# Optimization experiments

Hardware: AMD Instinct MI355X
Metric: run time of the kernel (lower is better)

The kernel has to match this reference:

```python
import jax, jax.numpy as jnp
import numpy as np

HID = 16
DATA_DIM = 2
B = 2048
T = 64
RTOL, ATOL = 1e-2, 1e-4
SAFETY, FMIN, FMAX = 0.9, 0.2, 10.0
MAX_STEPS = 16  # bounded adaptive-step budget (masked once t reaches T1)
T1 = 1.0
DT0 = 1.0

# Tsit5 (Tsitouras 2011) tableau
_A2 = (0.161,)
_A3 = (-0.008480655492356989, 0.335480655492357)
_A4 = (2.8971530571054935, -6.359448489975075, 4.3622954328695815)
_A5 = (5.325864828439257, -11.748883564062828, 7.4955393428898365, -0.09249506636175525)
_A6 = (5.86145544294642, -12.92096931784711, 8.159367898576159, -0.071584973281401, -0.028269050394068383)
_B5 = (0.09646076681806523, 0.01, 0.4798896504144996, 1.379008574103742, -3.290069515436081, 2.324710524099774)
_BT = (-0.00178001105222577714, -0.0008164344596567469, 0.007880878010261995, -0.1447110071732629, 0.5823571654525552, -0.45808210592918697, 0.015151515151515152)


def setup_inputs() -> dict:
    key = jax.random.key(0)
    ks = jax.random.split(key, 13)
    u = lambda k, shape, fan: jax.random.uniform(k, shape, jnp.float32, -1.0, 1.0) / np.float32(np.sqrt(fan))
    return dict(
        x_seq=jax.random.normal(ks[0], (B, T, DATA_DIM), jnp.float32),
        w1=u(ks[1], (HID, HID), HID), b1=u(ks[2], (HID,), HID),
        w2=u(ks[3], (HID, HID), HID), b2=u(ks[4], (HID,), HID),
        w3=u(ks[5], (HID, HID), HID), b3=u(ks[6], (HID,), HID),
        gru_wih=u(ks[7], (3 * HID, DATA_DIM), DATA_DIM),
        gru_whh=u(ks[8], (3 * HID, HID), HID),
        gru_b=u(ks[9], (3 * HID,), HID),
        gru_bn=u(ks[10], (HID,), HID),
        pred_w=u(ks[11], (1, HID), HID),
        pred_b=u(ks[12], (1,), HID),
    )


def _mlp(y, w1, b1, w2, b2, w3, b3):
    # eqx.nn.MLP(in=16, out=16, width=16, depth=2, activation=tanh): 3 Linear layers
    y = jnp.tanh(y @ w1.T + b1)
    y = jnp.tanh(y @ w2.T + b2)
    return y @ w3.T + b3


def _ode_solve(h0, f):
    """Adaptive Tsit5 + I-controller (diffrax PIDController defaults) from t=0 to t=1.
    Per-sample adaptive step/accept/reject, batched over the leading axis."""
    nB = h0.shape[0]

    def body(state, _):
        y, t, dt = state                      # y:[B,16]  t,dt:[B]
        dt_c = jnp.minimum(dt, T1 - t)        # clip so we never overshoot t1
        d = dt_c[:, None]
        k1 = f(y)
        k2 = f(y + d * (_A2[0] * k1))
        k3 = f(y + d * (_A3[0] * k1 + _A3[1] * k2))
        k4 = f(y + d * (_A4[0] * k1 + _A4[1] * k2 + _A4[2] * k3))
        k5 = f(y + d * (_A5[0] * k1 + _A5[1] * k2 + _A5[2] * k3 + _A5[3] * k4))
        k6 = f(y + d * (_A6[0] * k1 + _A6[1] * k2 + _A6[2] * k3 + _A6[3] * k4 + _A6[4] * k5))
        y_new = y + d * (_B5[0] * k1 + _B5[1] * k2 + _B5[2] * k3 + _B5[3] * k4 + _B5[4] * k5 + _B5[5] * k6)
        k7 = f(y_new)                          # FSAL stage, enters only the error estimate
        err = d * (_BT[0] * k1 + _BT[1] * k2 + _BT[2] * k3 + _BT[3] * k4 + _BT[4] * k5 + _BT[5] * k6 + _BT[6] * k7)
        scale = ATOL + RTOL * jnp.maximum(jnp.abs(y), jnp.abs(y_new))
        err2 = jnp.maximum(jnp.mean((err / scale) ** 2, axis=-1), 1e-16)  # squared RMS norm, [B]
        accept = err2 <= 1.0
        y = jnp.where(accept[:, None], y_new, y)
        t = jnp.where(accept, t + dt_c, t)
        # I-controller: factor = safety * err_norm**(-1/order), order=5
        factor = jnp.clip(SAFETY * err2 ** (-0.1), FMIN, FMAX)
        dt = dt_c * factor
        return (y, t, dt), None

    init = (h0, jnp.zeros((nB,), h0.dtype), jnp.full((nB,), DT0, h0.dtype))
    (y, _, _), _ = jax.lax.scan(body, init, None, length=MAX_STEPS)
    return y


def _gru(x, h, wih, whh, b, bn):
    # eqx.nn.GRUCell math
    ig = x @ wih.T + b
    hg = h @ whh.T
    ir, iz, inn = jnp.split(ig, 3, axis=-1)
    hr, hz, hn = jnp.split(hg, 3, axis=-1)
    r = jax.nn.sigmoid(ir + hr)
    z = jax.nn.sigmoid(iz + hz)
    n = jnp.tanh(inn + r * (hn + bn))
    return n + z * (h - n)


def reference(x_seq, w1, b1, w2, b2, w3, b3, gru_wih, gru_whh, gru_b, gru_bn, pred_w, pred_b):
    f = lambda y: _mlp(y, w1, b1, w2, b2, w3, b3)
    h0 = jnp.zeros((x_seq.shape[0], HID), x_seq.dtype)

    def step(h, x_t):
        h_ev = _ode_solve(h, f)
        h_new = _gru(x_t, h_ev, gru_wih, gru_whh, gru_b, gru_bn)
        return h_new, None

    xs = jnp.swapaxes(x_seq, 0, 1)  # [T, B, D]
    h_final, _ = jax.lax.scan(step, h0, xs)
    return h_final @ pred_w.T + pred_b  # [B, 1]
```

## Files before the change

### kernel.cpp

```cpp
#include <hip/hip_runtime.h>


#define T_STEPS 64
#define NB 2048
#define N_ODE_STEPS 16

typedef float v2f __attribute__((ext_vector_type(2)));

__device__ __forceinline__ v2f make2(float a, float b) { v2f r; r.x = a; r.y = b; return r; }

#define ROR(x, r) __int_as_float(__builtin_amdgcn_update_dpp( \
    0, __float_as_int(x), 0x120 + (r), 0xF, 0xF, true))

__device__ __forceinline__ float rsum16(float v) {
  v += ROR(v, 8);
  v += ROR(v, 4);
  v += ROR(v, 2);
  v += ROR(v, 1);
  return v;
}

__constant__ int PR_[8] = {0, 2, 4, 6, 1, 3, 5, 7};

__device__ __forceinline__ void gather8(float y, v2f (&G)[4]) {
  float r0 = y;
  float r4 = ROR(r0, 4);
  float r2 = ROR(r0, 2);
  float r6 = ROR(r4, 2);
  float r1 = ROR(r0, 1);
  float r3 = ROR(r2, 1);
  float r5 = ROR(r4, 1);
  float r7 = ROR(r6, 1);
  G[0] = make2(r0, r2);
  G[1] = make2(r4, r6);
  G[2] = make2(r1, r3);
  G[3] = make2(r5, r7);
}

__device__ __forceinline__ float dotAB(const v2f (&WA)[4], const v2f (&WB)[4],
                                       const v2f (&G)[4], float bias) {
  v2f a0 = __builtin_elementwise_fma(G[0], WA[0], make2(bias, 0.0f));
  v2f a1 = G[1] * WA[1];
  v2f b0 = G[0] * WB[0];
  v2f b1 = G[1] * WB[1];
  a0 = __builtin_elementwise_fma(G[2], WA[2], a0);
  a1 = __builtin_elementwise_fma(G[3], WA[3], a1);
  b0 = __builtin_elementwise_fma(G[2], WB[2], b0);
  b1 = __builtin_elementwise_fma(G[3], WB[3], b1);
  v2f as = a0 + a1;
  v2f bs = b0 + b1;
  float bsc = bs.x + bs.y;
  float bsw = ROR(bsc, 8);
  return (as.x + as.y) + bsw;
}

__device__ __forceinline__ float fast_tanh(float x) {
  float e = __builtin_amdgcn_exp2f(x * 2.885390081777927f);
  return fmaf(-2.0f, __builtin_amdgcn_rcpf(e + 1.0f), 1.0f);
}

__device__ __forceinline__ float sigmoid_(float x) {
  float e = __builtin_amdgcn_exp2f(x * -1.4426950408889634f);
  return __builtin_amdgcn_rcpf(1.0f + e);
}

__device__ __forceinline__ float mlp_f(float u,
    const v2f (&w1a)[4], const v2f (&w1b)[4], float b1v,
    const v2f (&w2a)[4], const v2f (&w2b)[4], float b2v,
    const v2f (&w3a)[4], const v2f (&w3b)[4], float b3v) {
  v2f G[4];
  gather8(u, G);
  float h1 = fast_tanh(dotAB(w1a, w1b, G, b1v));
  gather8(h1, G);
  float h2 = fast_tanh(dotAB(w2a, w2b, G, b2v));
  gather8(h2, G);
  return dotAB(w3a, w3b, G, b3v);
}

__global__
__attribute__((amdgpu_flat_work_group_size(64, 64), amdgpu_waves_per_eu(1, 1)))
void odern_kernel(
    const float* __restrict__ x_seq,
    const float* __restrict__ w1, const float* __restrict__ b1,
    const float* __restrict__ w2, const float* __restrict__ b2,
    const float* __restrict__ w3, const float* __restrict__ b3,
    const float* __restrict__ gru_wih, const float* __restrict__ gru_whh,
    const float* __restrict__ gru_b, const float* __restrict__ gru_bn,
    const float* __restrict__ pred_w, const float* __restrict__ pred_b,
    float* __restrict__ out) {
  const int tid = threadIdx.x;
  const int j = tid & 15;
  const int g = tid >> 4;
  const int b = blockIdx.x * 4 + g;
  const int jj = (j + 8) & 15;

  v2f w1a[4], w1b[4], w2a[4], w2b[4], w3a[4], w3b[4];
  v2f wha[4], whb[4], wza[4], wzb[4], wna[4], wnb[4];
#pragma unroll
  for (int p = 0; p < 4; ++p) {
    const int ia = (j - PR_[2 * p]) & 15;
    const int ib = (j - PR_[2 * p + 1]) & 15;
    w1a[p] = make2(w1[j * 16 + ia],  w1[j * 16 + ib]);
    w1b[p] = make2(w1[jj * 16 + ia], w1[jj * 16 + ib]);
    w2a[p] = make2(w2[j * 16 + ia],  w2[j * 16 + ib]);
    w2b[p] = make2(w2[jj * 16 + ia], w2[jj * 16 + ib]);
    w3a[p] = make2(w3[j * 16 + ia],  w3[j * 16 + ib]);
    w3b[p] = make2(w3[jj * 16 + ia], w3[jj * 16 + ib]);
    wha[p] = make2(gru_whh[j * 16 + ia],         gru_whh[j * 16 + ib]);
    whb[p] = make2(gru_whh[jj * 16 + ia],        gru_whh[jj * 16 + ib]);
    wza[p] = make2(gru_whh[(16 + j) * 16 + ia],  gru_whh[(16 + j) * 16 + ib]);
    wzb[p] = make2(gru_whh[(16 + jj) * 16 + ia], gru_whh[(16 + jj) * 16 + ib]);
    wna[p] = make2(gru_whh[(32 + j) * 16 + ia],  gru_whh[(32 + j) * 16 + ib]);
    wnb[p] = make2(gru_whh[(32 + jj) * 16 + ia], gru_whh[(32 + jj) * 16 + ib]);
  }
  const float b1v = b1[j], b2v = b2[j], b3v = b3[j];
  const float wih_r0 = gru_wih[j * 2],        wih_r1 = gru_wih[j * 2 + 1];
  const float wih_z0 = gru_wih[(16 + j) * 2], wih_z1 = gru_wih[(16 + j) * 2 + 1];
  const float wih_n0 = gru_wih[(32 + j) * 2], wih_n1 = gru_wih[(32 + j) * 2 + 1];
  const float gb_r = gru_b[j], gb_z = gru_b[16 + j], gb_n = gru_b[32 + j];
  const float bnv = gru_bn[j];
  const float pwv = pred_w[j], pbv = pred_b[0];

  const float* xp = x_seq + (size_t)b * (T_STEPS * 2);

  float h = 0.0f;
#pragma unroll 1
  for (int t = 0; t < T_STEPS; ++t) {
    const float x0 = xp[2 * t];
    const float x1 = xp[2 * t + 1];

    float y = h;
    float tt = 0.0f, dt = 1.0f;
    float k1 = mlp_f(y, w1a, w1b, b1v, w2a, w2b, b2v, w3a, w3b, b3v);
#pragma unroll 1
    for (int s = 0; s < N_ODE_STEPS; ++s) {
      if (__all(tt >= 1.0f)) break;

      const float dt_c = fminf(dt, 1.0f - tt);
      const float d = dt_c;

      float s2 = 0.161f * k1;
      float k2 = mlp_f(fmaf(d, s2, y), w1a, w1b, b1v, w2a, w2b, b2v, w3a, w3b, b3v);

      float s3 = fmaf(0.335480655492357f, k2, -0.008480655492356989f * k1);
      float k3 = mlp_f(fmaf(d, s3, y), w1a, w1b, b1v, w2a, w2b, b2v, w3a, w3b, b3v);

      float s4 = fmaf(4.3622954328695815f, k3,
                 fmaf(-6.359448489975075f, k2, 2.8971530571054935f * k1));
      float k4 = mlp_f(fmaf(d, s4, y), w1a, w1b, b1v, w2a, w2b, b2v, w3a, w3b, b3v);

      float s5 = fmaf(-0.09249506636175525f, k4,
                 fmaf(7.4955393428898365f, k3,
                 fmaf(-11.748883564062828f, k2, 5.325864828439257f * k1)));
      float k5 = mlp_f(fmaf(d, s5, y), w1a, w1b, b1v, w2a, w2b, b2v, w3a, w3b, b3v);

      float s6 = fmaf(-0.028269050394068383f, k5,
                 fmaf(-0.071584973281401f, k4,
                 fmaf(8.159367898576159f, k3,
                 fmaf(-12.92096931784711f, k2, 5.86145544294642f * k1))));
      float k6 = mlp_f(fmaf(d, s6, y), w1a, w1b, b1v, w2a, w2b, b2v, w3a, w3b, b3v);

      float sy = fmaf(2.324710524099774f, k6,
                 fmaf(-3.290069515436081f, k5,
                 fmaf(1.379008574103742f, k4,
                 fmaf(0.4798896504144996f, k3,
                 fmaf(0.01f, k2, 0.09646076681806523f * k1)))));
      float y_new = fmaf(d, sy, y);

      float k7 = mlp_f(y_new, w1a, w1b, b1v, w2a, w2b, b2v, w3a, w3b, b3v);

      float se = fmaf(0.015151515151515152f, k7,
                 fmaf(-0.45808210592918697f, k6,
                 fmaf(0.5823571654525552f, k5,
                 fmaf(-0.1447110071732629f, k4,
                 fmaf(0.007880878010261995f, k3,
                 fmaf(-0.0008164344596567469f, k2, -0.001780011052225777f * k1))))));
      float err = d * se;

      float scale = fmaf(0.01f, fmaxf(fabsf(y), fabsf(y_new)), 0.0001f);
      float r = err * __builtin_amdgcn_rcpf(scale);
      float m = rsum16(r * r) * 0.0625f;
      float err2 = fmaxf(m, 1e-16f);

      const bool acc = err2 <= 1.0f;
      y = acc ? y_new : y;
      tt = acc ? tt + dt_c : tt;
      k1 = acc ? k7 : k1;

      float fac = 0.9f * __builtin_amdgcn_exp2f(-0.1f * __builtin_amdgcn_logf(err2));
      fac = fminf(fmaxf(fac, 0.2f), 10.0f);
      dt = dt_c * fac;
    }

    float ir = fmaf(wih_r1, x1, fmaf(wih_r0, x0, gb_r));
    float iz = fmaf(wih_z1, x1, fmaf(wih_z0, x0, gb_z));
    float in_ = fmaf(wih_n1, x1, fmaf(wih_n0, x0, gb_n));
    v2f G[4];
    gather8(y, G);
    float pre_r = dotAB(wha, whb, G, ir);
    float pre_z = dotAB(wza, wzb, G, iz);
    float hnb   = dotAB(wna, wnb, G, bnv);
    float rg = sigmoid_(pre_r);
    float zg = sigmoid_(pre_z);
    float ng = fast_tanh(fmaf(rg, hnb, in_));
    h = fmaf(zg, y - ng, ng);
  }

  float ps = rsum16(h * pwv);
  if (j == 0) out[b] = ps + pbv;
}

extern "C" void kernel_launch(void* const* d_in, const int* in_sizes, int n_in,
                              void* d_out, int out_size, void* d_ws, size_t ws_size,
                              hipStream_t stream) {
  (void)in_sizes; (void)n_in; (void)out_size; (void)d_ws; (void)ws_size;
  odern_kernel<<<dim3(NB / 4), dim3(64), 0, stream>>>(
      (const float*)d_in[0],
      (const float*)d_in[1], (const float*)d_in[2],
      (const float*)d_in[3], (const float*)d_in[4],
      (const float*)d_in[5], (const float*)d_in[6],
      (const float*)d_in[7], (const float*)d_in[8],
      (const float*)d_in[9], (const float*)d_in[10],
      (const float*)d_in[11], (const float*)d_in[12],
      (float*)d_out);
}
```

Baseline: 177.2 us.

## Split each sample's hidden dot products across two wave halves via permlane32 swap

Each sample now occupies 32 lanes instead of 16, so every lane does half of each 16-wide dot product (4 gathered inputs instead of 8). The halves are combined with a permlane32 swap and a DPP row rotate, and biases are zeroed on the upper half. The grid doubles to 1024 blocks of two samples each. This shortens the per-lane serial chain of DPP gathers and FMAs on the latency-bound ODE path, at the cost of twice as many waves and extra cross-half exchange instructions.

```diff
diff --git a/kernel.cpp b/kernel.cpp
--- a/kernel.cpp
+++ b/kernel.cpp
@@ -6,11 +6,15 @@
 #define N_ODE_STEPS 16
 
 typedef float v2f __attribute__((ext_vector_type(2)));
+typedef int v2i __attribute__((ext_vector_type(2)));
 
 __device__ __forceinline__ v2f make2(float a, float b) { v2f r; r.x = a; r.y = b; return r; }
 
 #define ROR(x, r) __int_as_float(__builtin_amdgcn_update_dpp( \
     0, __float_as_int(x), 0x120 + (r), 0xF, 0xF, true))
+
+#define ROR4_HI(x) __int_as_float(__builtin_amdgcn_update_dpp( \
+    __float_as_int(x), __float_as_int(x), 0x124, 0xC, 0xF, false))
 
 __device__ __forceinline__ float rsum16(float v) {
   v += ROR(v, 8);
@@ -20,38 +24,37 @@
   return v;
 }
 
-__constant__ int PR_[8] = {0, 2, 4, 6, 1, 3, 5, 7};
-
-__device__ __forceinline__ void gather8(float y, v2f (&G)[4]) {
-  float r0 = y;
-  float r4 = ROR(r0, 4);
-  float r2 = ROR(r0, 2);
-  float r6 = ROR(r4, 2);
-  float r1 = ROR(r0, 1);
+__device__ __forceinline__ float xhalf_sum(float part) {
+  v2i pr = __builtin_amdgcn_permlane32_swap(
+      __float_as_int(part), __float_as_int(part), false, false);
+  return __int_as_float(pr[0]) + __int_as_float(pr[1]);
+}
+
+struct G2 { v2f a, b; };
+
+__device__ __forceinline__ G2 gather4(float x) {
+  float r1 = ROR(x, 1);
+  float r2 = ROR(x, 2);
   float r3 = ROR(r2, 1);
-  float r5 = ROR(r4, 1);
-  float r7 = ROR(r6, 1);
-  G[0] = make2(r0, r2);
-  G[1] = make2(r4, r6);
-  G[2] = make2(r1, r3);
-  G[3] = make2(r5, r7);
-}
-
-__device__ __forceinline__ float dotAB(const v2f (&WA)[4], const v2f (&WB)[4],
-                                       const v2f (&G)[4], float bias) {
-  v2f a0 = __builtin_elementwise_fma(G[0], WA[0], make2(bias, 0.0f));
-  v2f a1 = G[1] * WA[1];
-  v2f b0 = G[0] * WB[0];
-  v2f b1 = G[1] * WB[1];
-  a0 = __builtin_elementwise_fma(G[2], WA[2], a0);
-  a1 = __builtin_elementwise_fma(G[3], WA[3], a1);
-  b0 = __builtin_elementwise_fma(G[2], WB[2], b0);
-  b1 = __builtin_elementwise_fma(G[3], WB[3], b1);
-  v2f as = a0 + a1;
-  v2f bs = b0 + b1;
-  float bsc = bs.x + bs.y;
-  float bsw = ROR(bsc, 8);
-  return (as.x + as.y) + bsw;
+  G2 g; g.a = make2(x, r1); g.b = make2(r2, r3); return g;
+}
+
+__device__ __forceinline__ float dotG(const v2f (&WA)[2], const v2f (&WB)[2],
+                                      const G2& g, float seed) {
+  v2f aa = __builtin_elementwise_fma(g.a, WA[0], make2(seed, 0.0f));
+  v2f bb = g.a * WB[0];
+  aa = __builtin_elementwise_fma(g.b, WA[1], aa);
+  bb = __builtin_elementwise_fma(g.b, WB[1], bb);
+  float a  = aa.x + aa.y;
+  float bs = bb.x + bb.y;
+  float part = a + ROR(bs, 8);
+  return ROR4_HI(xhalf_sum(part));
+}
+
+__device__ __forceinline__ float dotAB(const v2f (&WA)[2], const v2f (&WB)[2],
+                                       float x, float seed) {
+  G2 g = gather4(x);
+  return dotG(WA, WB, g, seed);
 }
 
 __device__ __forceinline__ float fast_tanh(float x) {
@@ -65,16 +68,12 @@
 }
 
 __device__ __forceinline__ float mlp_f(float u,
-    const v2f (&w1a)[4], const v2f (&w1b)[4], float b1v,
-    const v2f (&w2a)[4], const v2f (&w2b)[4], float b2v,
-    const v2f (&w3a)[4], const v2f (&w3b)[4], float b3v) {
-  v2f G[4];
-  gather8(u, G);
-  float h1 = fast_tanh(dotAB(w1a, w1b, G, b1v));
-  gather8(h1, G);
-  float h2 = fast_tanh(dotAB(w2a, w2b, G, b2v));
-  gather8(h2, G);
-  return dotAB(w3a, w3b, G, b3v);
+    const v2f (&w1a)[2], const v2f (&w1b)[2], float b1s,
+    const v2f (&w2a)[2], const v2f (&w2b)[2], float b2s,
+    const v2f (&w3a)[2], const v2f (&w3b)[2], float b3s) {
+  float h1 = fast_tanh(dotAB(w1a, w1b, u, b1s));
+  float h2 = fast_tanh(dotAB(w2a, w2b, h1, b2s));
+  return dotAB(w3a, w3b, h2, b3s);
 }
 
 __global__
@@ -90,48 +89,58 @@
     float* __restrict__ out) {
   const int tid = threadIdx.x;
   const int j = tid & 15;
-  const int g = tid >> 4;
-  const int b = blockIdx.x * 4 + g;
+  const int row16 = tid >> 4;
+  const int smp = row16 & 1;
+  const int hf = row16 >> 1;
+  const int b = blockIdx.x * 2 + smp;
   const int jj = (j + 8) & 15;
-
-  v2f w1a[4], w1b[4], w2a[4], w2b[4], w3a[4], w3b[4];
-  v2f wha[4], whb[4], wza[4], wzb[4], wna[4], wnb[4];
+  const int base = (j - 4 * hf) & 15;
+
+  v2f w1a[2], w1b[2], w2a[2], w2b[2], w3a[2], w3b[2];
+  v2f wha[2], whb[2], wza[2], wzb[2], wna[2], wnb[2];
 #pragma unroll
-  for (int p = 0; p < 4; ++p) {
-    const int ia = (j - PR_[2 * p]) & 15;
-    const int ib = (j - PR_[2 * p + 1]) & 15;
-    w1a[p] = make2(w1[j * 16 + ia],  w1[j * 16 + ib]);
-    w1b[p] = make2(w1[jj * 16 + ia], w1[jj * 16 + ib]);
-    w2a[p] = make2(w2[j * 16 + ia],  w2[j * 16 + ib]);
-    w2b[p] = make2(w2[jj * 16 + ia], w2[jj * 16 + ib]);
-    w3a[p] = make2(w3[j * 16 + ia],  w3[j * 16 + ib]);
-    w3b[p] = make2(w3[jj * 16 + ia], w3[jj * 16 + ib]);
-    wha[p] = make2(gru_whh[j * 16 + ia],         gru_whh[j * 16 + ib]);
-    whb[p] = make2(gru_whh[jj * 16 + ia],        gru_whh[jj * 16 + ib]);
-    wza[p] = make2(gru_whh[(16 + j) * 16 + ia],  gru_whh[(16 + j) * 16 + ib]);
-    wzb[p] = make2(gru_whh[(16 + jj) * 16 + ia], gru_whh[(16 + jj) * 16 + ib]);
-    wna[p] = make2(gru_whh[(32 + j) * 16 + ia],  gru_whh[(32 + j) * 16 + ib]);
-    wnb[p] = make2(gru_whh[(32 + jj) * 16 + ia], gru_whh[(32 + jj) * 16 + ib]);
+  for (int p = 0; p < 2; ++p) {
+    const int ca = (base - 2 * p) & 15;
+    const int cb = (base - 2 * p - 1) & 15;
+    w1a[p] = make2(w1[j * 16 + ca],  w1[j * 16 + cb]);
+    w1b[p] = make2(w1[jj * 16 + ca], w1[jj * 16 + cb]);
+    w2a[p] = make2(w2[j * 16 + ca],  w2[j * 16 + cb]);
+    w2b[p] = make2(w2[jj * 16 + ca], w2[jj * 16 + cb]);
+    w3a[p] = make2(w3[j * 16 + ca],  w3[j * 16 + cb]);
+    w3b[p] = make2(w3[jj * 16 + ca], w3[jj * 16 + cb]);
+    wha[p] = make2(gru_whh[j * 16 + ca],         gru_whh[j * 16 + cb]);
+    whb[p] = make2(gru_whh[jj * 16 + ca],        gru_whh[jj * 16 + cb]);
+    wza[p] = make2(gru_whh[(16 + j) * 16 + ca],  gru_whh[(16 + j) * 16 + cb]);
+    wzb[p] = make2(gru_whh[(16 + jj) * 16 + ca], gru_whh[(16 + jj) * 16 + cb]);
+    wna[p] = make2(gru_whh[(32 + j) * 16 + ca],  gru_whh[(32 + j) * 16 + cb]);
+    wnb[p] = make2(gru_whh[(32 + jj) * 16 + ca], gru_whh[(32 + jj) * 16 + cb]);
   }
-  const float b1v = b1[j], b2v = b2[j], b3v = b3[j];
-  const float wih_r0 = gru_wih[j * 2],        wih_r1 = gru_wih[j * 2 + 1];
-  const float wih_z0 = gru_wih[(16 + j) * 2], wih_z1 = gru_wih[(16 + j) * 2 + 1];
-  const float wih_n0 = gru_wih[(32 + j) * 2], wih_n1 = gru_wih[(32 + j) * 2 + 1];
-  const float gb_r = gru_b[j], gb_z = gru_b[16 + j], gb_n = gru_b[32 + j];
-  const float bnv = gru_bn[j];
-  const float pwv = pred_w[j], pbv = pred_b[0];
+  const float b1s = hf ? 0.0f : b1[j];
+  const float b2s = hf ? 0.0f : b2[j];
+  const float b3s = hf ? 0.0f : b3[j];
+  const float wih_r0 = hf ? 0.0f : gru_wih[j * 2];
+  const float wih_r1 = hf ? 0.0f : gru_wih[j * 2 + 1];
+  const float wih_z0 = hf ? 0.0f : gru_wih[(16 + j) * 2];
+  const float wih_z1 = hf ? 0.0f : gru_wih[(16 + j) * 2 + 1];
+  const float gb_r = hf ? 0.0f : gru_b[j];
+  const float gb_z = hf ? 0.0f : gru_b[16 + j];
+  const float bns  = hf ? 0.0f : gru_bn[j];
+  const float wih_n0 = gru_wih[(32 + base) * 2];
+  const float wih_n1 = gru_wih[(32 + base) * 2 + 1];
+  const float gb_n = gru_b[32 + base];
+  const float pwv = pred_w[base], pbv = pred_b[0];
 
   const float* xp = x_seq + (size_t)b * (T_STEPS * 2);
 
-  float h = 0.0f;
+  float hst = 0.0f;
 #pragma unroll 1
   for (int t = 0; t < T_STEPS; ++t) {
     const float x0 = xp[2 * t];
     const float x1 = xp[2 * t + 1];
 
-    float y = h;
+    float y = hst;
     float tt = 0.0f, dt = 1.0f;
-    float k1 = mlp_f(y, w1a, w1b, b1v, w2a, w2b, b2v, w3a, w3b, b3v);
+    float k1 = mlp_f(y, w1a, w1b, b1s, w2a, w2b, b2s, w3a, w3b, b3s);
 #pragma unroll 1
     for (int s = 0; s < N_ODE_STEPS; ++s) {
       if (__all(tt >= 1.0f)) break;
@@ -140,25 +149,25 @@
       const float d = dt_c;
 
       float s2 = 0.161f * k1;
-      float k2 = mlp_f(fmaf(d, s2, y), w1a, w1b, b1v, w2a, w2b, b2v, w3a, w3b, b3v);
+      float k2 = mlp_f(fmaf(d, s2, y), w1a, w1b, b1s, w2a, w2b, b2s, w3a, w3b, b3s);
 
       float s3 = fmaf(0.335480655492357f, k2, -0.008480655492356989f * k1);
-      float k3 = mlp_f(fmaf(d, s3, y), w1a, w1b, b1v, w2a, w2b, b2v, w3a, w3b, b3v);
+      float k3 = mlp_f(fmaf(d, s3, y), w1a, w1b, b1s, w2a, w2b, b2s, w3a, w3b, b3s);
 
       float s4 = fmaf(4.3622954328695815f, k3,
                  fmaf(-6.359448489975075f, k2, 2.8971530571054935f * k1));
-      float k4 = mlp_f(fmaf(d, s4, y), w1a, w1b, b1v, w2a, w2b, b2v, w3a, w3b, b3v);
+      float k4 = mlp_f(fmaf(d, s4, y), w1a, w1b, b1s, w2a, w2b, b2s, w3a, w3b, b3s);
 
       float s5 = fmaf(-0.09249506636175525f, k4,
                  fmaf(7.4955393428898365f, k3,
                  fmaf(-11.748883564062828f, k2, 5.325864828439257f * k1)));
-      float k5 = mlp_f(fmaf(d, s5, y), w1a, w1b, b1v, w2a, w2b, b2v, w3a, w3b, b3v);
+      float k5 = mlp_f(fmaf(d, s5, y), w1a, w1b, b1s, w2a, w2b, b2s, w3a, w3b, b3s);
 
       float s6 = fmaf(-0.028269050394068383f, k5,
                  fmaf(-0.071584973281401f, k4,
                  fmaf(8.159367898576159f, k3,
                  fmaf(-12.92096931784711f, k2, 5.86145544294642f * k1))));
-      float k6 = mlp_f(fmaf(d, s6, y), w1a, w1b, b1v, w2a, w2b, b2v, w3a, w3b, b3v);
+      float k6 = mlp_f(fmaf(d, s6, y), w1a, w1b, b1s, w2a, w2b, b2s, w3a, w3b, b3s);
 
       float sy = fmaf(2.324710524099774f, k6,
                  fmaf(-3.290069515436081f, k5,
@@ -167,7 +176,7 @@
                  fmaf(0.01f, k2, 0.09646076681806523f * k1)))));
       float y_new = fmaf(d, sy, y);
 
-      float k7 = mlp_f(y_new, w1a, w1b, b1v, w2a, w2b, b2v, w3a, w3b, b3v);
+      float k7 = mlp_f(y_new, w1a, w1b, b1s, w2a, w2b, b2s, w3a, w3b, b3s);
 
       float se = fmaf(0.015151515151515152f, k7,
                  fmaf(-0.45808210592918697f, k6,
@@ -192,29 +201,28 @@
       dt = dt_c * fac;
     }
 
-    float ir = fmaf(wih_r1, x1, fmaf(wih_r0, x0, gb_r));
-    float iz = fmaf(wih_z1, x1, fmaf(wih_z0, x0, gb_z));
+    float ir  = fmaf(wih_r1, x1, fmaf(wih_r0, x0, gb_r));
+    float iz  = fmaf(wih_z1, x1, fmaf(wih_z0, x0, gb_z));
     float in_ = fmaf(wih_n1, x1, fmaf(wih_n0, x0, gb_n));
-    v2f G[4];
-    gather8(y, G);
-    float pre_r = dotAB(wha, whb, G, ir);
-    float pre_z = dotAB(wza, wzb, G, iz);
-    float hnb   = dotAB(wna, wnb, G, bnv);
+    G2 gy = gather4(y);
+    float pre_r = dotG(wha, whb, gy, ir);
+    float pre_z = dotG(wza, wzb, gy, iz);
+    float hnb   = dotG(wna, wnb, gy, bns);
     float rg = sigmoid_(pre_r);
     float zg = sigmoid_(pre_z);
     float ng = fast_tanh(fmaf(rg, hnb, in_));
-    h = fmaf(zg, y - ng, ng);
+    hst = fmaf(zg, y - ng, ng);
   }
 
-  float ps = rsum16(h * pwv);
-  if (j == 0) out[b] = ps + pbv;
+  float ps = rsum16(hst * pwv);
+  if (hf == 0 && j == 0) out[b] = ps + pbv;
 }
 
 extern "C" void kernel_launch(void* const* d_in, const int* in_sizes, int n_in,
                               void* d_out, int out_size, void* d_ws, size_t ws_size,
                               hipStream_t stream) {
   (void)in_sizes; (void)n_in; (void)out_size; (void)d_ws; (void)ws_size;
-  odern_kernel<<<dim3(NB / 4), dim3(64), 0, stream>>>(
+  odern_kernel<<<dim3(NB / 2), dim3(64), 0, stream>>>(
       (const float*)d_in[0],
       (const float*)d_in[1], (const float*)d_in[2],
       (const float*)d_in[3], (const float*)d_in[4],
```

After: 171.6 us. 1.03x faster.
